# Kernel optimization log

Hardware: AMD Instinct MI355X
Metric: run time of the kernel (lower is better)

The kernel has to match this reference:

```python
import jax, jax.numpy as jnp
import numpy as np

EMBED_DIM = 512
NUM_HEAD = 16
HEAD_DIM = EMBED_DIM // NUM_HEAD
EPS = 1e-6


def setup_inputs() -> dict:
    key = jax.random.key(0)
    ks = jax.random.split(key, 7)
    B, L = 4, 4096
    scale = 1.0 / np.sqrt(EMBED_DIM)
    return {
        "query": jax.random.normal(ks[0], (B, L, EMBED_DIM), jnp.float32),
        "key": jax.random.normal(ks[1], (B, L, EMBED_DIM), jnp.float32),
        "value": jax.random.normal(ks[2], (B, L, EMBED_DIM), jnp.float32),
        "Wq": jax.random.normal(ks[3], (EMBED_DIM, EMBED_DIM), jnp.float32) * scale,
        "Wk": jax.random.normal(ks[4], (EMBED_DIM, EMBED_DIM), jnp.float32) * scale,
        "Wv": jax.random.normal(ks[5], (EMBED_DIM, EMBED_DIM), jnp.float32) * scale,
        "Wm": jax.random.normal(ks[6], (EMBED_DIM, EMBED_DIM), jnp.float32) * scale,
    }


def reference(query, key, value, Wq, Wk, Wv, Wm):
    bs, Lq, E = query.shape
    H, D = NUM_HEAD, HEAD_DIM
    # projections (nn.Linear without bias: x @ W.T)
    q = (query @ Wq.T).reshape(bs, Lq, H, D)
    k = (key @ Wk.T).reshape(bs, -1, H, D)
    v = (value @ Wv.T).reshape(bs, -1, H, D)
    # elu+1 feature map
    Q = jax.nn.elu(q) + 1.0
    K = jax.nn.elu(k) + 1.0
    v_len = v.shape[1]
    v = v / v_len
    # KV accumulation: [n, h, d, dv]
    KV = jnp.einsum('nshd,nshv->nhdv', K, v)
    # normalizer Z: [n, l, h]
    Z = 1.0 / (jnp.einsum('nlhd,nhd->nlh', Q, K.sum(axis=1)) + EPS)
    # weighted combination: [n, l, h, dv]
    message = jnp.einsum('nlhd,nhdv,nlh->nlhv', Q, KV, Z) * v_len
    # merge projection (dropout p=0 -> identity)
    out = message.reshape(bs, Lq, H * D) @ Wm.T
    return out
```

## Files before the change

kernel.cpp:

```cpp
#include <hip/hip_runtime.h>

#define EMBED  512
#define NHEAD  16
#define HDIM   32
#define NBATCH 4
#define SEQ    4096
#define NROWS  (NBATCH * SEQ)
#define NE     (NROWS * EMBED)
#define WN     (EMBED * EMBED)
#define FEPS   1e-6f

typedef __attribute__((ext_vector_type(8))) short short8;
typedef __attribute__((ext_vector_type(4))) float f32x4;

__device__ __forceinline__ short f2bf(float x) {
    unsigned u = __float_as_uint(x);
    u += 0x7FFFu + ((u >> 16) & 1u);
    return (short)(u >> 16);
}
__device__ __forceinline__ float bf2f(short h) {
    return __uint_as_float(((unsigned)(unsigned short)h) << 16);
}

#define GLDS16(gp, lp)                                                   \
    __builtin_amdgcn_global_load_lds(                                    \
        (__attribute__((address_space(1))) void*)(void*)(gp),            \
        (__attribute__((address_space(3))) void*)(void*)(lp), 16, 0, 0)

__global__ __launch_bounds__(256)
void convert_all(const float* __restrict__ q, const float* __restrict__ k,
                 const float* __restrict__ v,
                 const float* __restrict__ wq, const float* __restrict__ wk,
                 const float* __restrict__ wv, const float* __restrict__ wm,
                 short* __restrict__ qh, short* __restrict__ ql,
                 short* __restrict__ kh, short* __restrict__ kl,
                 short* __restrict__ vh, short* __restrict__ vl,
                 short* __restrict__ wqh, short* __restrict__ wql,
                 short* __restrict__ wkh, short* __restrict__ wkl,
                 short* __restrict__ wvh, short* __restrict__ wvl,
                 short* __restrict__ wmh, short* __restrict__ wml) {
    const int b = blockIdx.x;
    const float* src; short* dh; short* dl; int boff;
    if (b < 12288) {
        const int s = b >> 12;
        src = (s == 0) ? q  : (s == 1) ? k  : v;
        dh  = (s == 0) ? qh : (s == 1) ? kh : vh;
        dl  = (s == 0) ? ql : (s == 1) ? kl : vl;
        boff = b & 4095;
    } else {
        const int s = (b - 12288) >> 7;
        src = (s == 0) ? wq  : (s == 1) ? wk  : (s == 2) ? wv  : wm;
        dh  = (s == 0) ? wqh : (s == 1) ? wkh : (s == 2) ? wvh : wmh;
        dl  = (s == 0) ? wql : (s == 1) ? wkl : (s == 2) ? wvl : wml;
        boff = (b - 12288) & 127;
    }
    const size_t i = ((size_t)boff * 256 + threadIdx.x) * 8;
    float4 x0 = *(const float4*)(src + i);
    float4 x1 = *(const float4*)(src + i + 4);
    float vv[8] = {x0.x, x0.y, x0.z, x0.w, x1.x, x1.y, x1.z, x1.w};
    short8 h, l;
#pragma unroll
    for (int t = 0; t < 8; ++t) {
        short hb = f2bf(vv[t]);
        h[t] = hb;
        l[t] = f2bf(vv[t] - bf2f(hb));
    }
    *(short8*)(dh + i) = h;
    *(short8*)(dl + i) = l;
}

__device__ __forceinline__ void gemm_core(
    const short* __restrict__ Ahp, const short* __restrict__ Alp,
    const short* __restrict__ Bhp, const short* __restrict__ Blp,
    int bmG, int bnG, short (*lds)[24576], f32x4 acc[4][4])
{
    const int tid  = threadIdx.x;
    const int lane = tid & 63;
    const int wave = tid >> 6;
    const int l15  = lane & 15;
    const int kg   = lane >> 4;

    const int sc8 = (((lane & 3) ^ ((lane >> 3) & 3)) << 3);
    const size_t aR0 = (size_t)(bmG + wave * 32 + (lane >> 2)) * EMBED + sc8;
    const size_t bR0 = (size_t)(bnG + wave * 16 + (lane >> 2)) * EMBED + sc8;

    const int dA = wave * 1024;
    const int dB = wave * 512;

    const int rk8   = ((kg ^ ((l15 >> 1) & 3)) << 3);
    const int aBase = ((wave >> 1) * 64 + l15) * 32 + rk8;
    const int bBase = 16384 + ((wave & 1) * 64 + l15) * 32 + rk8;

#pragma unroll
    for (int v = 0; v < 2; ++v) {
        short* T = lds[v];
        const int kp = v * 32;
        GLDS16(Ahp + aR0 + kp,              T + dA);
        GLDS16(Ahp + aR0 + 16 * EMBED + kp, T + dA + 512);
        GLDS16(Alp + aR0 + kp,              T + 8192 + dA);
        GLDS16(Alp + aR0 + 16 * EMBED + kp, T + 8192 + dA + 512);
        GLDS16(Bhp + bR0 + kp,              T + 16384 + dB);
        GLDS16(Blp + bR0 + kp,              T + 20480 + dB);
    }

    int rs = 0;
#pragma unroll 1
    for (int s = 0; s < 16; ++s) {
        if (s < 15) asm volatile("s_waitcnt vmcnt(6)" ::: "memory");
        else        asm volatile("s_waitcnt vmcnt(0)" ::: "memory");
        __builtin_amdgcn_s_barrier();
        __builtin_amdgcn_sched_barrier(0);

        short* S = lds[rs];
        short8 fah[4], fal[4], fbh[4], fbl[4];
#pragma unroll
        for (int f = 0; f < 4; ++f) {
            fah[f] = *(const short8*)(S + aBase + f * 512);
            fal[f] = *(const short8*)(S + 8192 + aBase + f * 512);
            fbh[f] = *(const short8*)(S + bBase + f * 512);
            fbl[f] = *(const short8*)(S + 4096 + bBase + f * 512);
        }
        if (s < 14) {
            const int ws2 = (rs + 2 >= 3) ? (rs - 1) : (rs + 2);
            short* T = lds[ws2];
            const int kp = (s + 2) * 32;
            GLDS16(Ahp + aR0 + kp,              T + dA);
            GLDS16(Ahp + aR0 + 16 * EMBED + kp, T + dA + 512);
            GLDS16(Alp + aR0 + kp,              T + 8192 + dA);
            GLDS16(Alp + aR0 + 16 * EMBED + kp, T + 8192 + dA + 512);
            GLDS16(Bhp + bR0 + kp,              T + 16384 + dB);
            GLDS16(Blp + bR0 + kp,              T + 20480 + dB);
        }
        __builtin_amdgcn_s_setprio(1);
#pragma unroll
        for (int i = 0; i < 4; ++i)
#pragma unroll
            for (int j = 0; j < 4; ++j) {
                acc[i][j] = __builtin_amdgcn_mfma_f32_16x16x32_bf16(fah[i], fbh[j], acc[i][j], 0, 0, 0);
                acc[i][j] = __builtin_amdgcn_mfma_f32_16x16x32_bf16(fah[i], fbl[j], acc[i][j], 0, 0, 0);
                acc[i][j] = __builtin_amdgcn_mfma_f32_16x16x32_bf16(fal[i], fbh[j], acc[i][j], 0, 0, 0);
            }
        __builtin_amdgcn_s_setprio(0);
        rs = (rs == 2) ? 0 : rs + 1;
    }
}

__global__ __launch_bounds__(512, 2)
void qkv_gemm(const short* __restrict__ Aqh, const short* __restrict__ Aql,
              const short* __restrict__ Akh, const short* __restrict__ Akl,
              const short* __restrict__ Avh, const short* __restrict__ Avl,
              const short* __restrict__ WqH, const short* __restrict__ WqL,
              const short* __restrict__ WkH, const short* __restrict__ WkL,
              const short* __restrict__ WvH, const short* __restrict__ WvL,
              float* __restrict__ Qb, float* __restrict__ Kb,
              float* __restrict__ Vb) {
    __shared__ short lds[3][24576];

    const int lin = blockIdx.x;
    const int op  = lin >> 8;
    const int r_  = lin & 255;
    const int bnG = ((r_ >> 6) & 3) * 128;
    const int bmG = (r_ & 63) * 256;

    const short* Ah = (op == 0) ? Aqh : (op == 1) ? Akh : Avh;
    const short* Al = (op == 0) ? Aql : (op == 1) ? Akl : Avl;
    const short* Bh = (op == 0) ? WqH : (op == 1) ? WkH : WvH;
    const short* Bl = (op == 0) ? WqL : (op == 1) ? WkL : WvL;
    float* C = (op == 0) ? Qb : (op == 1) ? Kb : Vb;

    f32x4 acc[4][4];
#pragma unroll
    for (int i = 0; i < 4; ++i)
#pragma unroll
        for (int j = 0; j < 4; ++j) acc[i][j] = (f32x4)0.0f;

    gemm_core(Ah, Al, Bh, Bl, bmG, bnG, lds, acc);

    const int lane = threadIdx.x & 63;
    const int wave = threadIdx.x >> 6;
    const int l15  = lane & 15;
    const int kg   = lane >> 4;
    const int wm   = (wave >> 1) * 64;
    const int wn   = (wave & 1) * 64;
#pragma unroll
    for (int i = 0; i < 4; ++i)
#pragma unroll
        for (int j = 0; j < 4; ++j) {
            const int col = bnG + wn + j * 16 + l15;
#pragma unroll
            for (int r = 0; r < 4; ++r) {
                const int row = bmG + wm + i * 16 + kg * 4 + r;
                float vv = acc[i][j][r];
                if (op < 2) vv = (vv > 0.f) ? (vv + 1.f) : __expf(vv);
                else        vv = vv * (1.0f / (float)SEQ);
                C[(size_t)row * EMBED + col] = vv;
            }
        }
}

__global__ __launch_bounds__(512, 2)
void merge_gemm(const short* __restrict__ Mh, const short* __restrict__ Ml,
                const short* __restrict__ WhP, const short* __restrict__ WlP,
                float* __restrict__ C) {
    __shared__ short lds[3][24576];

    const int lin = blockIdx.x;
    const int bnG = ((lin >> 6) & 3) * 128;
    const int bmG = (lin & 63) * 256;

    f32x4 acc[4][4];
#pragma unroll
    for (int i = 0; i < 4; ++i)
#pragma unroll
        for (int j = 0; j < 4; ++j) acc[i][j] = (f32x4)0.0f;

    gemm_core(Mh, Ml, WhP, WlP, bmG, bnG, lds, acc);

    const int lane = threadIdx.x & 63;
    const int wave = threadIdx.x >> 6;
    const int l15  = lane & 15;
    const int kg   = lane >> 4;
    const int wm   = (wave >> 1) * 64;
    const int wn   = (wave & 1) * 64;
#pragma unroll
    for (int i = 0; i < 4; ++i)
#pragma unroll
        for (int j = 0; j < 4; ++j) {
            const int col = bnG + wn + j * 16 + l15;
#pragma unroll
            for (int r = 0; r < 4; ++r) {
                const int row = bmG + wm + i * 16 + kg * 4 + r;
                C[(size_t)row * EMBED + col] = acc[i][j][r];
            }
        }
}

__global__ __launch_bounds__(256)
void kv_ksum_mfma(const float* __restrict__ Kf, const float* __restrict__ Vf,
                  float* __restrict__ KV, float* __restrict__ Ksum) {
    __shared__ char smem[34816];
    short (*Kh)[34] = (short (*)[34])smem;
    short (*Kl)[34] = (short (*)[34])(smem + 8704);
    short (*Vh)[34] = (short (*)[34])(smem + 17408);
    short (*Vl)[34] = (short (*)[34])(smem + 26112);

    const int bh_ = blockIdx.y;
    const int b = bh_ >> 4, h = bh_ & 15;
    const int s0 = blockIdx.x * 256;
    const int t = threadIdx.x;
    const int lane = t & 63, wave = t >> 6;
    const int l15 = lane & 15, kg = lane >> 4;
    const int ws = wave * 32;

    const int sl = t >> 1;
    const int dsel = (t & 1) * 16;
    const float* Kbase = Kf + (size_t)b * SEQ * EMBED + h * HDIM;
    const float* Vbase = Vf + (size_t)b * SEQ * EMBED + h * HDIM;

    f32x4 kvacc[2][2], ksacc[2];
#pragma unroll
    for (int i = 0; i < 2; ++i) {
        ksacc[i] = (f32x4)0.0f;
#pragma unroll
        for (int j = 0; j < 2; ++j) kvacc[i][j] = (f32x4)0.0f;
    }
    short8 ones;
#pragma unroll
    for (int q = 0; q < 8; ++q) ones[q] = (short)0x3F80;

    float4 kx[4], vx[4];
#pragma unroll
    for (int p = 0; p < 4; ++p) {
        kx[p] = *(const float4*)(Kbase + (size_t)(s0 + sl) * EMBED + dsel + 4 * p);
        vx[p] = *(const float4*)(Vbase + (size_t)(s0 + sl) * EMBED + dsel + 4 * p);
    }

#pragma unroll 1
    for (int it = 0; it < 2; ++it) {
        __syncthreads();
        {
            float kv_[8] = {kx[0].x, kx[0].y, kx[0].z, kx[0].w, kx[1].x, kx[1].y, kx[1].z, kx[1].w};
            float kv2[8] = {kx[2].x, kx[2].y, kx[2].z, kx[2].w, kx[3].x, kx[3].y, kx[3].z, kx[3].w};
            float vv_[8] = {vx[0].x, vx[0].y, vx[0].z, vx[0].w, vx[1].x, vx[1].y, vx[1].z, vx[1].w};
            float vv2[8] = {vx[2].x, vx[2].y, vx[2].z, vx[2].w, vx[3].x, vx[3].y, vx[3].z, vx[3].w};
            short8 h0, l0, h1, l1;
#pragma unroll
            for (int q = 0; q < 8; ++q) { short hb = f2bf(kv_[q]); h0[q] = hb; l0[q] = f2bf(kv_[q] - bf2f(hb)); }
#pragma unroll
            for (int q = 0; q < 8; ++q) { short hb = f2bf(kv2[q]); h1[q] = hb; l1[q] = f2bf(kv2[q] - bf2f(hb)); }
            *(short8*)&Kh[sl][dsel] = h0; *(short8*)&Kh[sl][dsel + 8] = h1;
            *(short8*)&Kl[sl][dsel] = l0; *(short8*)&Kl[sl][dsel + 8] = l1;
#pragma unroll
            for (int q = 0; q < 8; ++q) { short hb = f2bf(vv_[q]); h0[q] = hb; l0[q] = f2bf(vv_[q] - bf2f(hb)); }
#pragma unroll
            for (int q = 0; q < 8; ++q) { short hb = f2bf(vv2[q]); h1[q] = hb; l1[q] = f2bf(vv2[q] - bf2f(hb)); }
            *(short8*)&Vh[sl][dsel] = h0; *(short8*)&Vh[sl][dsel + 8] = h1;
            *(short8*)&Vl[sl][dsel] = l0; *(short8*)&Vl[sl][dsel + 8] = l1;
        }
        __syncthreads();
        if (it == 0) {
#pragma unroll
            for (int p = 0; p < 4; ++p) {
                kx[p] = *(const float4*)(Kbase + (size_t)(s0 + 128 + sl) * EMBED + dsel + 4 * p);
                vx[p] = *(const float4*)(Vbase + (size_t)(s0 + 128 + sl) * EMBED + dsel + 4 * p);
            }
        }
        short8 kah[2], kal[2], vbh[2], vbl[2];
#pragma unroll
        for (int i = 0; i < 2; ++i) {
#pragma unroll
            for (int q = 0; q < 8; ++q) {
                const int srow = ws + kg * 8 + q;
                const int col  = i * 16 + l15;
                kah[i][q] = Kh[srow][col];
                kal[i][q] = Kl[srow][col];
                vbh[i][q] = Vh[srow][col];
                vbl[i][q] = Vl[srow][col];
            }
        }
#pragma unroll
        for (int i = 0; i < 2; ++i) {
#pragma unroll
            for (int j = 0; j < 2; ++j) {
                kvacc[i][j] = __builtin_amdgcn_mfma_f32_16x16x32_bf16(kah[i], vbh[j], kvacc[i][j], 0, 0, 0);
                kvacc[i][j] = __builtin_amdgcn_mfma_f32_16x16x32_bf16(kah[i], vbl[j], kvacc[i][j], 0, 0, 0);
                kvacc[i][j] = __builtin_amdgcn_mfma_f32_16x16x32_bf16(kal[i], vbh[j], kvacc[i][j], 0, 0, 0);
            }
            ksacc[i] = __builtin_amdgcn_mfma_f32_16x16x32_bf16(kah[i], ones, ksacc[i], 0, 0, 0);
            ksacc[i] = __builtin_amdgcn_mfma_f32_16x16x32_bf16(kal[i], ones, ksacc[i], 0, 0, 0);
        }
    }

    __syncthreads();
    float* red = (float*)smem;
    float* myred = red + wave * 1056;
#pragma unroll
    for (int i = 0; i < 2; ++i)
#pragma unroll
        for (int j = 0; j < 2; ++j)
#pragma unroll
            for (int r = 0; r < 4; ++r)
                myred[(i * 16 + kg * 4 + r) * 32 + j * 16 + l15] = kvacc[i][j][r];
    if (l15 == 0) {
#pragma unroll
        for (int i = 0; i < 2; ++i)
#pragma unroll
            for (int r = 0; r < 4; ++r)
                myred[1024 + i * 16 + kg * 4 + r] = ksacc[i][r];
    }
    __syncthreads();
    float* kvout = KV + (size_t)bh_ * 1024;
    for (int idx = t; idx < 1024; idx += 256) {
        float s4 = red[idx] + red[1056 + idx] + red[2112 + idx] + red[3168 + idx];
        atomicAdd(&kvout[idx], s4);
    }
    if (t < 32) {
        float s4 = red[1024 + t] + red[1056 + 1024 + t] + red[2112 + 1024 + t] + red[3168 + 1024 + t];
        atomicAdd(&Ksum[bh_ * 32 + t], s4);
    }
}

__global__ __launch_bounds__(512)
void message_kernel(const float* __restrict__ Q, const float* __restrict__ KV,
                    const float* __restrict__ Ksum,
                    short* __restrict__ Mh, short* __restrict__ Ml) {
    const int blk  = blockIdx.x;
    const int row0 = blk * 4;
    const int b    = row0 >> 12;
    const int t    = threadIdx.x;
    const int h    = t >> 5, e = t & 31;

    __shared__ float q[4][EMBED];
    __shared__ float ks[EMBED];
    ks[t] = Ksum[b * EMBED + t];
#pragma unroll
    for (int r = 0; r < 4; ++r) q[r][t] = Q[(size_t)(row0 + r) * EMBED + t];

    const float* kvh = KV + (size_t)(b * NHEAD + h) * HDIM * HDIM + e;
    float kc[HDIM];
#pragma unroll
    for (int d = 0; d < HDIM; ++d) kc[d] = kvh[d * HDIM];
    __syncthreads();

#pragma unroll
    for (int r = 0; r < 4; ++r) {
        float zden = FEPS, m = 0.f;
#pragma unroll
        for (int d = 0; d < HDIM; ++d) {
            float qd = q[r][h * HDIM + d];
            zden = fmaf(qd, ks[h * HDIM + d], zden);
            m    = fmaf(qd, kc[d], m);
        }
        float vv = m * ((float)SEQ / zden);
        short hb = f2bf(vv);
        Mh[(size_t)(row0 + r) * EMBED + t] = hb;
        Ml[(size_t)(row0 + r) * EMBED + t] = f2bf(vv - bf2f(hb));
    }
}

extern "C" void kernel_launch(void* const* d_in, const int* in_sizes, int n_in,
                              void* d_out, int out_size, void* d_ws, size_t ws_size,
                              hipStream_t stream) {
    const float* query = (const float*)d_in[0];
    const float* key   = (const float*)d_in[1];
    const float* value = (const float*)d_in[2];
    const float* Wq    = (const float*)d_in[3];
    const float* Wk    = (const float*)d_in[4];
    const float* Wv    = (const float*)d_in[5];
    const float* Wm    = (const float*)d_in[6];
    float* out = (float*)d_out;

    float* ws  = (float*)d_ws;
    float* Qb  = ws;
    float* Kb  = Qb + (size_t)NE;
    float* Vb  = Kb + (size_t)NE;
    float* KVb = Vb + (size_t)NE;
    float* KSb = KVb + 64 * 1024;
    short* wsp = (short*)(KSb + 64 * HDIM);
    short* WqH = wsp;            short* WqL = wsp + WN;
    short* WkH = wsp + 2 * WN;   short* WkL = wsp + 3 * WN;
    short* WvH = wsp + 4 * WN;   short* WvL = wsp + 5 * WN;
    short* WmH = wsp + 6 * WN;   short* WmL = wsp + 7 * WN;
    short* Xp  = wsp + 8 * WN;
    short* Qih = Xp;             short* Qil = Xp + (size_t)NE;
    short* Kih = Xp + 2 * (size_t)NE;  short* Kil = Xp + 3 * (size_t)NE;
    short* Vih = Xp + 4 * (size_t)NE;  short* Vil = Xp + 5 * (size_t)NE;
    short* Mh = (short*)Kb;
    short* Ml = Mh + (size_t)NE;

    hipMemsetAsync(KVb, 0, (64 * 1024 + 64 * HDIM) * sizeof(float), stream);

    convert_all<<<12800, 256, 0, stream>>>(query, key, value, Wq, Wk, Wv, Wm,
                                           Qih, Qil, Kih, Kil, Vih, Vil,
                                           WqH, WqL, WkH, WkL,
                                           WvH, WvL, WmH, WmL);

    qkv_gemm<<<768, 512, 0, stream>>>(Qih, Qil, Kih, Kil, Vih, Vil,
                                      WqH, WqL, WkH, WkL, WvH, WvL,
                                      Qb, Kb, Vb);

    kv_ksum_mfma<<<dim3(16, 64), 256, 0, stream>>>(Kb, Vb, KVb, KSb);
    message_kernel<<<NROWS / 4, 512, 0, stream>>>(Qb, KVb, KSb, Mh, Ml);

    merge_gemm<<<256, 512, 0, stream>>>(Mh, Ml, WmH, WmL, out);
}
```

Baseline: 303.1 us.

## Replace LDS-staged GEMM with direct global fragment loads and fuse split conversions

The GEMM core drops LDS staging with global_load_lds and triple buffering. Each wave now loads its MFMA fragments straight from global memory with register double-buffering, using 256-thread blocks, 128x128 tiles and an XCD-aware block remap. The QKV GEMM epilogue writes K and V already split into bf16 hi/lo pairs, so kv_ksum no longer converts fp32, and the KV/Ksum zeroing moves into extra convert_all blocks in place of a memset. Without LDS sharing, each block reads fragments redundantly from global memory and relies on L2 hit rates, and the scattered short stores in the epilogue may be poorly coalesced.

```diff
diff --git a/kernel.cpp b/kernel.cpp
--- a/kernel.cpp
+++ b/kernel.cpp
@@ -21,11 +21,6 @@
 __device__ __forceinline__ float bf2f(short h) {
     return __uint_as_float(((unsigned)(unsigned short)h) << 16);
 }
-
-#define GLDS16(gp, lp)                                                   \
-    __builtin_amdgcn_global_load_lds(                                    \
-        (__attribute__((address_space(1))) void*)(void*)(gp),            \
-        (__attribute__((address_space(3))) void*)(void*)(lp), 16, 0, 0)
 
 __global__ __launch_bounds__(256)
 void convert_all(const float* __restrict__ q, const float* __restrict__ k,
@@ -38,8 +33,16 @@
                  short* __restrict__ wqh, short* __restrict__ wql,
                  short* __restrict__ wkh, short* __restrict__ wkl,
                  short* __restrict__ wvh, short* __restrict__ wvl,
-                 short* __restrict__ wmh, short* __restrict__ wml) {
+                 short* __restrict__ wmh, short* __restrict__ wml,
+                 float* __restrict__ zeroDst) {
     const int b = blockIdx.x;
+    if (b >= 12800) {
+        const int nvec = (64 * 1024 + 64 * HDIM) / 4;
+        float4 z = {0.f, 0.f, 0.f, 0.f};
+        for (int i = (b - 12800) * 256 + threadIdx.x; i < nvec; i += 16 * 256)
+            ((float4*)zeroDst)[i] = z;
+        return;
+    }
     const float* src; short* dh; short* dl; int boff;
     if (b < 12288) {
         const int s = b >> 12;
@@ -69,104 +72,89 @@
     *(short8*)(dl + i) = l;
 }
 
-__device__ __forceinline__ void gemm_core(
-    const short* __restrict__ Ahp, const short* __restrict__ Alp,
-    const short* __restrict__ Bhp, const short* __restrict__ Blp,
-    int bmG, int bnG, short (*lds)[24576], f32x4 acc[4][4])
+__device__ __forceinline__ void ldfrag(
+    const short* __restrict__ pa, const short* __restrict__ pal,
+    const short* __restrict__ pb, const short* __restrict__ pbl, int ko,
+    short8 ah[4], short8 al[4], short8 bh[4], short8 bl[4])
 {
-    const int tid  = threadIdx.x;
-    const int lane = tid & 63;
-    const int wave = tid >> 6;
+#pragma unroll
+    for (int i = 0; i < 4; ++i) {
+        ah[i] = *(const short8*)(pa  + (size_t)i * 16 * EMBED + ko);
+        al[i] = *(const short8*)(pal + (size_t)i * 16 * EMBED + ko);
+        bh[i] = *(const short8*)(pb  + (size_t)i * 16 * EMBED + ko);
+        bl[i] = *(const short8*)(pbl + (size_t)i * 16 * EMBED + ko);
+    }
+}
+
+__device__ __forceinline__ void mfma48(
+    const short8 ah[4], const short8 al[4],
+    const short8 bh[4], const short8 bl[4], f32x4 acc[4][4])
+{
+#pragma unroll
+    for (int i = 0; i < 4; ++i)
+#pragma unroll
+        for (int j = 0; j < 4; ++j) {
+            acc[i][j] = __builtin_amdgcn_mfma_f32_16x16x32_bf16(ah[i], bh[j], acc[i][j], 0, 0, 0);
+            acc[i][j] = __builtin_amdgcn_mfma_f32_16x16x32_bf16(ah[i], bl[j], acc[i][j], 0, 0, 0);
+            acc[i][j] = __builtin_amdgcn_mfma_f32_16x16x32_bf16(al[i], bh[j], acc[i][j], 0, 0, 0);
+        }
+}
+
+__device__ __forceinline__ void gemm_direct(
+    const short* __restrict__ Ah, const short* __restrict__ Al,
+    const short* __restrict__ Bh, const short* __restrict__ Bl,
+    int bm, int bn, f32x4 acc[4][4])
+{
+    const int lane = threadIdx.x & 63;
+    const int wave = threadIdx.x >> 6;
     const int l15  = lane & 15;
     const int kg   = lane >> 4;
-
-    const int sc8 = (((lane & 3) ^ ((lane >> 3) & 3)) << 3);
-    const size_t aR0 = (size_t)(bmG + wave * 32 + (lane >> 2)) * EMBED + sc8;
-    const size_t bR0 = (size_t)(bnG + wave * 16 + (lane >> 2)) * EMBED + sc8;
-
-    const int dA = wave * 1024;
-    const int dB = wave * 512;
-
-    const int rk8   = ((kg ^ ((l15 >> 1) & 3)) << 3);
-    const int aBase = ((wave >> 1) * 64 + l15) * 32 + rk8;
-    const int bBase = 16384 + ((wave & 1) * 64 + l15) * 32 + rk8;
-
-#pragma unroll
-    for (int v = 0; v < 2; ++v) {
-        short* T = lds[v];
-        const int kp = v * 32;
-        GLDS16(Ahp + aR0 + kp,              T + dA);
-        GLDS16(Ahp + aR0 + 16 * EMBED + kp, T + dA + 512);
-        GLDS16(Alp + aR0 + kp,              T + 8192 + dA);
-        GLDS16(Alp + aR0 + 16 * EMBED + kp, T + 8192 + dA + 512);
-        GLDS16(Bhp + bR0 + kp,              T + 16384 + dB);
-        GLDS16(Blp + bR0 + kp,              T + 20480 + dB);
-    }
-
-    int rs = 0;
+    const int wm   = (wave >> 1) * 64;
+    const int wn   = (wave & 1) * 64;
+
+    const short* pa  = Ah + (size_t)(bm + wm + l15) * EMBED + kg * 8;
+    const short* pal = Al + (size_t)(bm + wm + l15) * EMBED + kg * 8;
+    const short* pb  = Bh + (size_t)(bn + wn + l15) * EMBED + kg * 8;
+    const short* pbl = Bl + (size_t)(bn + wn + l15) * EMBED + kg * 8;
+
+    short8 A0h[4], A0l[4], B0h[4], B0l[4];
+    short8 A1h[4], A1l[4], B1h[4], B1l[4];
+
+    ldfrag(pa, pal, pb, pbl, 0, A0h, A0l, B0h, B0l);
 #pragma unroll 1
-    for (int s = 0; s < 16; ++s) {
-        if (s < 15) asm volatile("s_waitcnt vmcnt(6)" ::: "memory");
-        else        asm volatile("s_waitcnt vmcnt(0)" ::: "memory");
-        __builtin_amdgcn_s_barrier();
-        __builtin_amdgcn_sched_barrier(0);
-
-        short* S = lds[rs];
-        short8 fah[4], fal[4], fbh[4], fbl[4];
-#pragma unroll
-        for (int f = 0; f < 4; ++f) {
-            fah[f] = *(const short8*)(S + aBase + f * 512);
-            fal[f] = *(const short8*)(S + 8192 + aBase + f * 512);
-            fbh[f] = *(const short8*)(S + bBase + f * 512);
-            fbl[f] = *(const short8*)(S + 4096 + bBase + f * 512);
-        }
-        if (s < 14) {
-            const int ws2 = (rs + 2 >= 3) ? (rs - 1) : (rs + 2);
-            short* T = lds[ws2];
-            const int kp = (s + 2) * 32;
-            GLDS16(Ahp + aR0 + kp,              T + dA);
-            GLDS16(Ahp + aR0 + 16 * EMBED + kp, T + dA + 512);
-            GLDS16(Alp + aR0 + kp,              T + 8192 + dA);
-            GLDS16(Alp + aR0 + 16 * EMBED + kp, T + 8192 + dA + 512);
-            GLDS16(Bhp + bR0 + kp,              T + 16384 + dB);
-            GLDS16(Blp + bR0 + kp,              T + 20480 + dB);
-        }
-        __builtin_amdgcn_s_setprio(1);
-#pragma unroll
-        for (int i = 0; i < 4; ++i)
-#pragma unroll
-            for (int j = 0; j < 4; ++j) {
-                acc[i][j] = __builtin_amdgcn_mfma_f32_16x16x32_bf16(fah[i], fbh[j], acc[i][j], 0, 0, 0);
-                acc[i][j] = __builtin_amdgcn_mfma_f32_16x16x32_bf16(fah[i], fbl[j], acc[i][j], 0, 0, 0);
-                acc[i][j] = __builtin_amdgcn_mfma_f32_16x16x32_bf16(fal[i], fbh[j], acc[i][j], 0, 0, 0);
-            }
-        __builtin_amdgcn_s_setprio(0);
-        rs = (rs == 2) ? 0 : rs + 1;
-    }
-}
-
-__global__ __launch_bounds__(512, 2)
+    for (int k0 = 0; k0 < EMBED - 64; k0 += 64) {
+        ldfrag(pa, pal, pb, pbl, k0 + 32, A1h, A1l, B1h, B1l);
+        mfma48(A0h, A0l, B0h, B0l, acc);
+        ldfrag(pa, pal, pb, pbl, k0 + 64, A0h, A0l, B0h, B0l);
+        mfma48(A1h, A1l, B1h, B1l, acc);
+    }
+    ldfrag(pa, pal, pb, pbl, EMBED - 32, A1h, A1l, B1h, B1l);
+    mfma48(A0h, A0l, B0h, B0l, acc);
+    mfma48(A1h, A1l, B1h, B1l, acc);
+}
+
+__global__ __launch_bounds__(256, 2)
 void qkv_gemm(const short* __restrict__ Aqh, const short* __restrict__ Aql,
               const short* __restrict__ Akh, const short* __restrict__ Akl,
               const short* __restrict__ Avh, const short* __restrict__ Avl,
               const short* __restrict__ WqH, const short* __restrict__ WqL,
               const short* __restrict__ WkH, const short* __restrict__ WkL,
               const short* __restrict__ WvH, const short* __restrict__ WvL,
-              float* __restrict__ Qb, float* __restrict__ Kb,
-              float* __restrict__ Vb) {
-    __shared__ short lds[3][24576];
-
+              float* __restrict__ Qb,
+              short* __restrict__ KhP, short* __restrict__ KlP,
+              short* __restrict__ VhP, short* __restrict__ VlP) {
     const int lin = blockIdx.x;
-    const int op  = lin >> 8;
-    const int r_  = lin & 255;
-    const int bnG = ((r_ >> 6) & 3) * 128;
-    const int bmG = (r_ & 63) * 256;
+    const int xcd = lin & 7;
+    const int w   = lin >> 3;
+    const int op  = w >> 6;
+    const int r   = w & 63;
+    const int bn  = (r & 3) * 128;
+    const int bm  = ((xcd << 4) + (r >> 2)) * 128;
 
     const short* Ah = (op == 0) ? Aqh : (op == 1) ? Akh : Avh;
     const short* Al = (op == 0) ? Aql : (op == 1) ? Akl : Avl;
     const short* Bh = (op == 0) ? WqH : (op == 1) ? WkH : WvH;
     const short* Bl = (op == 0) ? WqL : (op == 1) ? WkL : WvL;
-    float* C = (op == 0) ? Qb : (op == 1) ? Kb : Vb;
 
     f32x4 acc[4][4];
 #pragma unroll
@@ -174,7 +162,7 @@
 #pragma unroll
         for (int j = 0; j < 4; ++j) acc[i][j] = (f32x4)0.0f;
 
-    gemm_core(Ah, Al, Bh, Bl, bmG, bnG, lds, acc);
+    gemm_direct(Ah, Al, Bh, Bl, bm, bn, acc);
 
     const int lane = threadIdx.x & 63;
     const int wave = threadIdx.x >> 6;
@@ -182,31 +170,52 @@
     const int kg   = lane >> 4;
     const int wm   = (wave >> 1) * 64;
     const int wn   = (wave & 1) * 64;
-#pragma unroll
-    for (int i = 0; i < 4; ++i)
-#pragma unroll
-        for (int j = 0; j < 4; ++j) {
-            const int col = bnG + wn + j * 16 + l15;
-#pragma unroll
-            for (int r = 0; r < 4; ++r) {
-                const int row = bmG + wm + i * 16 + kg * 4 + r;
-                float vv = acc[i][j][r];
-                if (op < 2) vv = (vv > 0.f) ? (vv + 1.f) : __expf(vv);
-                else        vv = vv * (1.0f / (float)SEQ);
-                C[(size_t)row * EMBED + col] = vv;
+
+    if (op == 0) {
+#pragma unroll
+        for (int i = 0; i < 4; ++i)
+#pragma unroll
+            for (int j = 0; j < 4; ++j) {
+                const int col = bn + wn + j * 16 + l15;
+#pragma unroll
+                for (int rr = 0; rr < 4; ++rr) {
+                    const int row = bm + wm + i * 16 + kg * 4 + rr;
+                    float vv = acc[i][j][rr];
+                    vv = (vv > 0.f) ? (vv + 1.f) : __expf(vv);
+                    Qb[(size_t)row * EMBED + col] = vv;
+                }
             }
-        }
-}
-
-__global__ __launch_bounds__(512, 2)
+    } else {
+        short* Hp = (op == 1) ? KhP : VhP;
+        short* Lp = (op == 1) ? KlP : VlP;
+#pragma unroll
+        for (int i = 0; i < 4; ++i)
+#pragma unroll
+            for (int j = 0; j < 4; ++j) {
+                const int col = bn + wn + j * 16 + l15;
+#pragma unroll
+                for (int rr = 0; rr < 4; ++rr) {
+                    const int row = bm + wm + i * 16 + kg * 4 + rr;
+                    float vv = acc[i][j][rr];
+                    if (op == 1) vv = (vv > 0.f) ? (vv + 1.f) : __expf(vv);
+                    else         vv = vv * (1.0f / (float)SEQ);
+                    short hb = f2bf(vv);
+                    Hp[(size_t)row * EMBED + col] = hb;
+                    Lp[(size_t)row * EMBED + col] = f2bf(vv - bf2f(hb));
+                }
+            }
+    }
+}
+
+__global__ __launch_bounds__(256, 2)
 void merge_gemm(const short* __restrict__ Mh, const short* __restrict__ Ml,
                 const short* __restrict__ WhP, const short* __restrict__ WlP,
                 float* __restrict__ C) {
-    __shared__ short lds[3][24576];
-
     const int lin = blockIdx.x;
-    const int bnG = ((lin >> 6) & 3) * 128;
-    const int bmG = (lin & 63) * 256;
+    const int xcd = lin & 7;
+    const int w   = lin >> 3;
+    const int bn  = (w & 3) * 128;
+    const int bm  = ((xcd << 4) + (w >> 2)) * 128;
 
     f32x4 acc[4][4];
 #pragma unroll
@@ -214,7 +223,7 @@
 #pragma unroll
         for (int j = 0; j < 4; ++j) acc[i][j] = (f32x4)0.0f;
 
-    gemm_core(Mh, Ml, WhP, WlP, bmG, bnG, lds, acc);
+    gemm_direct(Mh, Ml, WhP, WlP, bm, bn, acc);
 
     const int lane = threadIdx.x & 63;
     const int wave = threadIdx.x >> 6;
@@ -226,17 +235,18 @@
     for (int i = 0; i < 4; ++i)
 #pragma unroll
         for (int j = 0; j < 4; ++j) {
-            const int col = bnG + wn + j * 16 + l15;
-#pragma unroll
-            for (int r = 0; r < 4; ++r) {
-                const int row = bmG + wm + i * 16 + kg * 4 + r;
-                C[(size_t)row * EMBED + col] = acc[i][j][r];
+            const int col = bn + wn + j * 16 + l15;
+#pragma unroll
+            for (int rr = 0; rr < 4; ++rr) {
+                const int row = bm + wm + i * 16 + kg * 4 + rr;
+                C[(size_t)row * EMBED + col] = acc[i][j][rr];
             }
         }
 }
 
 __global__ __launch_bounds__(256)
-void kv_ksum_mfma(const float* __restrict__ Kf, const float* __restrict__ Vf,
+void kv_ksum_mfma(const short* __restrict__ KhP, const short* __restrict__ KlP,
+                  const short* __restrict__ VhP, const short* __restrict__ VlP,
                   float* __restrict__ KV, float* __restrict__ Ksum) {
     __shared__ char smem[34816];
     short (*Kh)[34] = (short (*)[34])smem;
@@ -254,8 +264,7 @@
 
     const int sl = t >> 1;
     const int dsel = (t & 1) * 16;
-    const float* Kbase = Kf + (size_t)b * SEQ * EMBED + h * HDIM;
-    const float* Vbase = Vf + (size_t)b * SEQ * EMBED + h * HDIM;
+    const size_t rbase = (size_t)(b * SEQ + s0 + sl) * EMBED + h * HDIM + dsel;
 
     f32x4 kvacc[2][2], ksacc[2];
 #pragma unroll
@@ -268,42 +277,38 @@
 #pragma unroll
     for (int q = 0; q < 8; ++q) ones[q] = (short)0x3F80;
 
-    float4 kx[4], vx[4];
-#pragma unroll
-    for (int p = 0; p < 4; ++p) {
-        kx[p] = *(const float4*)(Kbase + (size_t)(s0 + sl) * EMBED + dsel + 4 * p);
-        vx[p] = *(const float4*)(Vbase + (size_t)(s0 + sl) * EMBED + dsel + 4 * p);
-    }
+    short8 pk[4], pv[4];
+    pk[0] = *(const short8*)(KhP + rbase);
+    pk[1] = *(const short8*)(KhP + rbase + 8);
+    pk[2] = *(const short8*)(KlP + rbase);
+    pk[3] = *(const short8*)(KlP + rbase + 8);
+    pv[0] = *(const short8*)(VhP + rbase);
+    pv[1] = *(const short8*)(VhP + rbase + 8);
+    pv[2] = *(const short8*)(VlP + rbase);
+    pv[3] = *(const short8*)(VlP + rbase + 8);
 
 #pragma unroll 1
     for (int it = 0; it < 2; ++it) {
         __syncthreads();
-        {
-            float kv_[8] = {kx[0].x, kx[0].y, kx[0].z, kx[0].w, kx[1].x, kx[1].y, kx[1].z, kx[1].w};
-            float kv2[8] = {kx[2].x, kx[2].y, kx[2].z, kx[2].w, kx[3].x, kx[3].y, kx[3].z, kx[3].w};
-            float vv_[8] = {vx[0].x, vx[0].y, vx[0].z, vx[0].w, vx[1].x, vx[1].y, vx[1].z, vx[1].w};
-            float vv2[8] = {vx[2].x, vx[2].y, vx[2].z, vx[2].w, vx[3].x, vx[3].y, vx[3].z, vx[3].w};
-            short8 h0, l0, h1, l1;
-#pragma unroll
-            for (int q = 0; q < 8; ++q) { short hb = f2bf(kv_[q]); h0[q] = hb; l0[q] = f2bf(kv_[q] - bf2f(hb)); }
-#pragma unroll
-            for (int q = 0; q < 8; ++q) { short hb = f2bf(kv2[q]); h1[q] = hb; l1[q] = f2bf(kv2[q] - bf2f(hb)); }
-            *(short8*)&Kh[sl][dsel] = h0; *(short8*)&Kh[sl][dsel + 8] = h1;
-            *(short8*)&Kl[sl][dsel] = l0; *(short8*)&Kl[sl][dsel + 8] = l1;
-#pragma unroll
-            for (int q = 0; q < 8; ++q) { short hb = f2bf(vv_[q]); h0[q] = hb; l0[q] = f2bf(vv_[q] - bf2f(hb)); }
-#pragma unroll
-            for (int q = 0; q < 8; ++q) { short hb = f2bf(vv2[q]); h1[q] = hb; l1[q] = f2bf(vv2[q] - bf2f(hb)); }
-            *(short8*)&Vh[sl][dsel] = h0; *(short8*)&Vh[sl][dsel + 8] = h1;
-            *(short8*)&Vl[sl][dsel] = l0; *(short8*)&Vl[sl][dsel + 8] = l1;
-        }
+        *(short8*)&Kh[sl][dsel]     = pk[0];
+        *(short8*)&Kh[sl][dsel + 8] = pk[1];
+        *(short8*)&Kl[sl][dsel]     = pk[2];
+        *(short8*)&Kl[sl][dsel + 8] = pk[3];
+        *(short8*)&Vh[sl][dsel]     = pv[0];
+        *(short8*)&Vh[sl][dsel + 8] = pv[1];
+        *(short8*)&Vl[sl][dsel]     = pv[2];
+        *(short8*)&Vl[sl][dsel + 8] = pv[3];
         __syncthreads();
         if (it == 0) {
-#pragma unroll
-            for (int p = 0; p < 4; ++p) {
-                kx[p] = *(const float4*)(Kbase + (size_t)(s0 + 128 + sl) * EMBED + dsel + 4 * p);
-                vx[p] = *(const float4*)(Vbase + (size_t)(s0 + 128 + sl) * EMBED + dsel + 4 * p);
-            }
+            const size_t rb2 = rbase + (size_t)128 * EMBED;
+            pk[0] = *(const short8*)(KhP + rb2);
+            pk[1] = *(const short8*)(KhP + rb2 + 8);
+            pk[2] = *(const short8*)(KlP + rb2);
+            pk[3] = *(const short8*)(KlP + rb2 + 8);
+            pv[0] = *(const short8*)(VhP + rb2);
+            pv[1] = *(const short8*)(VhP + rb2 + 8);
+            pv[2] = *(const short8*)(VlP + rb2);
+            pv[3] = *(const short8*)(VlP + rb2 + 8);
         }
         short8 kah[2], kal[2], vbh[2], vbl[2];
 #pragma unroll
@@ -412,9 +417,11 @@
 
     float* ws  = (float*)d_ws;
     float* Qb  = ws;
-    float* Kb  = Qb + (size_t)NE;
-    float* Vb  = Kb + (size_t)NE;
-    float* KVb = Vb + (size_t)NE;
+    short* KhP = (short*)(Qb + (size_t)NE);
+    short* KlP = KhP + (size_t)NE;
+    short* VhP = KhP + 2 * (size_t)NE;
+    short* VlP = KhP + 3 * (size_t)NE;
+    float* KVb = (float*)(KhP + 4 * (size_t)NE);
     float* KSb = KVb + 64 * 1024;
     short* wsp = (short*)(KSb + 64 * HDIM);
     short* WqH = wsp;            short* WqL = wsp + WN;
@@ -425,22 +432,20 @@
     short* Qih = Xp;             short* Qil = Xp + (size_t)NE;
     short* Kih = Xp + 2 * (size_t)NE;  short* Kil = Xp + 3 * (size_t)NE;
     short* Vih = Xp + 4 * (size_t)NE;  short* Vil = Xp + 5 * (size_t)NE;
-    short* Mh = (short*)Kb;
-    short* Ml = Mh + (size_t)NE;
-
-    hipMemsetAsync(KVb, 0, (64 * 1024 + 64 * HDIM) * sizeof(float), stream);
-
-    convert_all<<<12800, 256, 0, stream>>>(query, key, value, Wq, Wk, Wv, Wm,
+    short* Mh = Kih;
+    short* Ml = Kil;
+
+    convert_all<<<12816, 256, 0, stream>>>(query, key, value, Wq, Wk, Wv, Wm,
                                            Qih, Qil, Kih, Kil, Vih, Vil,
                                            WqH, WqL, WkH, WkL,
-                                           WvH, WvL, WmH, WmL);
-
-    qkv_gemm<<<768, 512, 0, stream>>>(Qih, Qil, Kih, Kil, Vih, Vil,
-                                      WqH, WqL, WkH, WkL, WvH, WvL,
-                                      Qb, Kb, Vb);
-
-    kv_ksum_mfma<<<dim3(16, 64), 256, 0, stream>>>(Kb, Vb, KVb, KSb);
+                                           WvH, WvL, WmH, WmL, KVb);
+
+    qkv_gemm<<<1536, 256, 0, stream>>>(Qih, Qil, Kih, Kil, Vih, Vil,
+                                       WqH, WqL, WkH, WkL, WvH, WvL,
+                                       Qb, KhP, KlP, VhP, VlP);
+
+    kv_ksum_mfma<<<dim3(16, 64), 256, 0, stream>>>(KhP, KlP, VhP, VlP, KVb, KSb);
     message_kernel<<<NROWS / 4, 512, 0, stream>>>(Qb, KVb, KSb, Mh, Ml);
 
-    merge_gemm<<<256, 512, 0, stream>>>(Mh, Ml, WmH, WmL, out);
-}
+    merge_gemm<<<512, 256, 0, stream>>>(Mh, Ml, WmH, WmL, out);
+}
```

After: 427.2 us. 1.41x slower.
